# Kernel optimization log

Hardware: AMD Instinct MI355X
Metric: run time of the kernel (lower is better)

Reference implementation:

```python
import jax, jax.numpy as jnp
import numpy as np

B, T, C, M = 64, 1024, 256, 1024  # note: broadcast in the torch source forces M == T


def setup_inputs() -> dict:
    key = jax.random.key(0)
    k = jax.random.split(key, 6)
    x = jax.random.normal(k[0], (B, T, C), jnp.float32)
    memory = 0.02 * jax.random.normal(k[1], (1, M, C), jnp.float32)  # nn.init.normal_(std=0.02)
    w1 = jax.random.normal(k[2], (2 * C, 4 * C), jnp.float32) / np.sqrt(2 * C)
    b1 = jnp.zeros((4 * C,), jnp.float32)
    w2 = jax.random.normal(k[3], (4 * C, C), jnp.float32) / np.sqrt(4 * C)
    b2 = jnp.zeros((C,), jnp.float32)
    return {"x": x, "memory": memory, "w1": w1, "b1": b1, "w2": w2, "b2": b2}


def reference(x, memory, w1, b1, w2, b2):
    # x: [B,T,C], memory: [1,M,C] (shared across batch, expanded lazily)
    mem = memory[0]                                        # [M,C]
    energy = jnp.einsum('btc,mc->btm', x, mem)             # cross-attn scores
    weights = jax.nn.softmax(energy, axis=-1)              # [B,T,M]
    retrieved = jnp.einsum('btm,mc->btc', weights, mem)    # [B,T,C]
    cat = jnp.concatenate([x, retrieved], axis=-1)         # [B,T,2C] (forward output)
    # gate MLP: Linear(2C,4C) -> SiLU -> Linear(4C,C) -> Sigmoid
    h = jax.nn.silu(jnp.einsum('btk,kf->btf', cat, w1) + b1)
    update_gate = jax.nn.sigmoid(jnp.einsum('btf,fc->btc', h, w2) + b2)  # [B,T,C], T==M
    # memory blend + batch-mean reduction (side-effect update in torch, detached)
    x_mean = jnp.mean(x, axis=1, keepdims=True)            # [B,1,C]
    new_mem = memory * (1.0 - update_gate) + x_mean * update_gate  # [B,M,C]
    new_memory = jnp.mean(new_mem, axis=0, keepdims=True)  # [1,M,C]
    return cat, new_memory
```

## Files before the change

### kernel.cpp

```cpp
#include <hip/hip_runtime.h>
#include <hip/hip_bf16.h>


#define BT 65536

typedef short bf16x8 __attribute__((ext_vector_type(8)));
typedef float f32x4 __attribute__((ext_vector_type(4)));

__device__ __forceinline__ unsigned short f2bf(float f) {
    unsigned x = __float_as_uint(f);
    unsigned r = (x + 0x7FFFu + ((x >> 16) & 1u)) >> 16;
    return (unsigned short)r;
}
__device__ __forceinline__ float bf2f(unsigned short u) {
    return __uint_as_float(((unsigned)u) << 16);
}

__device__ __forceinline__ void async16(const unsigned short* g, unsigned short* l) {
    __builtin_amdgcn_global_load_lds((const __attribute__((address_space(1))) unsigned int*)g,
                                     (__attribute__((address_space(3))) unsigned int*)l,
                                     16, 0, 0);
}


__global__ __launch_bounds__(256) void prep_x(const float* __restrict__ x,
                                              float* __restrict__ cat_out,
                                              unsigned short* __restrict__ cat_b) {
    long tid = (long)blockIdx.x * 256 + threadIdx.x;
    long i4 = tid * 4;
    long row = i4 >> 8;
    int c = (int)(i4 & 255);
    float4 v = *(const float4*)&x[i4];
    *(float4*)&cat_out[row * 512 + c] = v;
    ushort4 b4;
    b4.x = f2bf(v.x); b4.y = f2bf(v.y); b4.z = f2bf(v.z); b4.w = f2bf(v.w);
    *(ushort4*)&cat_b[row * 512 + c] = b4;
}

__global__ __launch_bounds__(256) void prep_mem(const float* __restrict__ mem,
                                                unsigned short* __restrict__ mem_b,
                                                unsigned short* __restrict__ memT_b) {
    int tid = blockIdx.x * 256 + threadIdx.x;
    mem_b[tid] = f2bf(mem[tid]);
    int c = tid >> 10, m = tid & 1023;
    memT_b[tid] = f2bf(mem[m * 256 + c]);
}

__global__ __launch_bounds__(256) void prep_w1(const float* __restrict__ w1,
                                               unsigned short* __restrict__ w1T) {
    int tid = blockIdx.x * 256 + threadIdx.x;
    int f = tid >> 9, k = tid & 511;
    w1T[tid] = f2bf(w1[k * 1024 + f]);
}

__global__ __launch_bounds__(256) void prep_w2(const float* __restrict__ w2,
                                               unsigned short* __restrict__ w2T) {
    int tid = blockIdx.x * 256 + threadIdx.x;
    int c = tid >> 10, k = tid & 1023;
    w2T[tid] = f2bf(w2[k * 256 + c]);
}

__global__ __launch_bounds__(256) void xmean_k(const float* __restrict__ x,
                                               float* __restrict__ xmean) {
    int b = blockIdx.x;
    int t0 = blockIdx.y * 64;
    int c = threadIdx.x;
    float s = 0.f;
    for (int t = 0; t < 64; t++)
        s += x[((long)(b * 1024 + t0 + t)) * 256 + c];
    atomicAdd(&xmean[b * 256 + c], s * (1.f / 1024.f));
}


__device__ __forceinline__ void compute_tile(const unsigned short* bufA,
                                             const unsigned short* bufB,
                                             const int* aoff, const int* boff,
                                             f32x4 acc[4][4]) {
    bf16x8 af[4], bfr[4];
#pragma unroll
    for (int i = 0; i < 4; i++) af[i] = *(const bf16x8*)&bufA[aoff[i]];
#pragma unroll
    for (int j = 0; j < 4; j++) bfr[j] = *(const bf16x8*)&bufB[boff[j]];
#pragma unroll
    for (int i = 0; i < 4; i++)
#pragma unroll
        for (int j = 0; j < 4; j++)
            acc[i][j] = __builtin_amdgcn_mfma_f32_16x16x32_bf16(af[i], bfr[j], acc[i][j], 0, 0, 0);
}

template <int MODE, int K>
__global__ __launch_bounds__(256) void gemm_bt(const unsigned short* __restrict__ A,
                                               const unsigned short* __restrict__ Bt,
                                               float* __restrict__ outF,
                                               unsigned short* __restrict__ outB,
                                               const float* __restrict__ bias) {
    constexpr long LDA = (MODE == 0 || MODE == 2) ? 512 : 1024;
    constexpr int NK = K / 32;
    const int t = threadIdx.x;
    const int wave = t >> 6, lane = t & 63;
    const int waveM = wave >> 1, waveN = wave & 1;
    const int quad = lane >> 4, l16 = lane & 15;

    const int nwg = gridDim.x * gridDim.y;
    const int lid = blockIdx.y * gridDim.x + blockIdx.x;
    const int sid = (lid & 7) * (nwg >> 3) + (lid >> 3);
    const int nb = sid % gridDim.x;
    const int mb = sid / gridDim.x;
    const long n0 = (long)nb * 128;
    const long m0 = (long)mb * 128;

    __shared__ unsigned short lA[3][128 * 32];
    __shared__ unsigned short lB[3][128 * 32];

    f32x4 acc[4][4] = {};

    const int sRow = wave * 16 + (lane >> 2);
    const int sC = (lane & 3) ^ ((sRow >> 1) & 3);
    const unsigned short* Ag0 = A + (m0 + sRow) * LDA + sC * 8;
    const unsigned short* Ag1 = Ag0 + 64 * LDA;
    const unsigned short* Bg0 = Bt + (n0 + sRow) * (long)K + sC * 8;
    const unsigned short* Bg1 = Bg0 + 64 * (long)K;
    const int so0 = wave * 512;
    const int so1 = 2048 + wave * 512;

    const int sx = (l16 >> 1) & 3;
    int aoff[4], boff[4];
#pragma unroll
    for (int i = 0; i < 4; i++) {
        aoff[i] = (waveM * 64 + i * 16 + l16) * 32 + ((quad ^ sx) * 8);
        boff[i] = (waveN * 64 + i * 16 + l16) * 32 + ((quad ^ sx) * 8);
    }

#define STAGE(BUF, KT) do {                                   \
        async16(Ag0 + (KT) * 32, &lA[BUF][so0]);              \
        async16(Ag1 + (KT) * 32, &lA[BUF][so1]);              \
        async16(Bg0 + (KT) * 32, &lB[BUF][so0]);              \
        async16(Bg1 + (KT) * 32, &lB[BUF][so1]);              \
    } while (0)

    STAGE(0, 0);
    STAGE(1, 1);
    asm volatile("s_waitcnt vmcnt(4)" ::: "memory");
    __builtin_amdgcn_s_barrier();
    __builtin_amdgcn_sched_barrier(0);

#pragma unroll
    for (int kt = 0; kt < NK; ++kt) {
        if (kt + 2 < NK) {
            STAGE((kt + 2) % 3, kt + 2);
            __builtin_amdgcn_sched_barrier(0);
        }
        compute_tile(&lA[kt % 3][0], &lB[kt % 3][0], aoff, boff, acc);
        if (kt + 2 < NK) {
            asm volatile("s_waitcnt vmcnt(4) lgkmcnt(0)" ::: "memory");
            __builtin_amdgcn_s_barrier();
            __builtin_amdgcn_sched_barrier(0);
        } else if (kt + 1 < NK) {
            asm volatile("s_waitcnt vmcnt(0) lgkmcnt(0)" ::: "memory");
            __builtin_amdgcn_s_barrier();
            __builtin_amdgcn_sched_barrier(0);
        }
    }
#undef STAGE

#pragma unroll
    for (int i = 0; i < 4; i++) {
#pragma unroll
        for (int j = 0; j < 4; j++) {
            long col = n0 + waveN * 64 + j * 16 + l16;
            float bval = (MODE == 2 || MODE == 3) ? bias[col] : 0.f;
#pragma unroll
            for (int r = 0; r < 4; r++) {
                long row = m0 + waveM * 64 + i * 16 + quad * 4 + r;
                float v = acc[i][j][r];
                if (MODE == 0) {
                    outB[row * 1024 + col] = f2bf(v);
                } else if (MODE == 1) {
                    long o = row * 512 + 256 + col;
                    outF[o] = v;
                    outB[o] = f2bf(v);
                } else if (MODE == 2) {
                    float z = v + bval;
                    float s = 1.f / (1.f + __expf(-z));
                    outB[row * 1024 + col] = f2bf(z * s);
                } else {
                    float z = v + bval;
                    outF[row * 256 + col] = 1.f / (1.f + __expf(-z));
                }
            }
        }
    }
}

__global__ __launch_bounds__(256) void softmax_rows(unsigned short* __restrict__ P) {
    long row = (long)blockIdx.x * 4 + (threadIdx.x >> 6);
    int lane = threadIdx.x & 63;
    unsigned short* p = P + row * 1024 + lane * 16;
    uint4 u0 = *(const uint4*)p;
    uint4 u1 = *(const uint4*)(p + 8);
    const unsigned short* ua = (const unsigned short*)&u0;
    const unsigned short* ub = (const unsigned short*)&u1;
    float v[16];
#pragma unroll
    for (int i = 0; i < 8; i++) { v[i] = bf2f(ua[i]); v[i + 8] = bf2f(ub[i]); }
    float m = -1e30f;
#pragma unroll
    for (int i = 0; i < 16; i++) m = fmaxf(m, v[i]);
    for (int off = 32; off >= 1; off >>= 1) m = fmaxf(m, __shfl_xor(m, off));
    float s = 0.f;
#pragma unroll
    for (int i = 0; i < 16; i++) { v[i] = __expf(v[i] - m); s += v[i]; }
    for (int off = 32; off >= 1; off >>= 1) s += __shfl_xor(s, off);
    float inv = 1.f / s;
    unsigned short o[16];
#pragma unroll
    for (int i = 0; i < 16; i++) o[i] = f2bf(v[i] * inv);
    *(uint4*)p = *(uint4*)&o[0];
    *(uint4*)(p + 8) = *(uint4*)&o[8];
}

__global__ __launch_bounds__(256) void reduce_mem(const float* __restrict__ gate,
                                                  const float* __restrict__ memory,
                                                  const float* __restrict__ xmean,
                                                  float* __restrict__ out2) {
    int m = blockIdx.x, c = threadIdx.x;
    float mm = memory[m * 256 + c];
    float s = 0.f;
    for (int b = 0; b < 64; b++)
        s += gate[((long)(b * 1024 + m)) * 256 + c] * (xmean[b * 256 + c] - mm);
    out2[m * 256 + c] = mm + s * (1.f / 64.f);
}

extern "C" void kernel_launch(void* const* d_in, const int* in_sizes, int n_in,
                              void* d_out, int out_size, void* d_ws, size_t ws_size,
                              hipStream_t stream) {
    const float* x      = (const float*)d_in[0];
    const float* memory = (const float*)d_in[1];
    const float* w1     = (const float*)d_in[2];
    const float* b1     = (const float*)d_in[3];
    const float* w2     = (const float*)d_in[4];
    const float* b2     = (const float*)d_in[5];
    float* out = (float*)d_out;

    unsigned short* mem_b  = (unsigned short*)d_ws;
    unsigned short* memT_b = mem_b + 262144;
    unsigned short* w1T    = memT_b + 262144;
    unsigned short* w2T    = w1T + 524288;
    float* xmean           = (float*)(w2T + 262144);
    unsigned short* cat_b  = (unsigned short*)(xmean + 16384);
    unsigned short* Pbuf   = cat_b + 33554432;
    float* gate            = (float*)cat_b;

    hipMemsetAsync(xmean, 0, 64 * 256 * sizeof(float), stream);

    prep_mem<<<1024, 256, 0, stream>>>(memory, mem_b, memT_b);
    prep_w1<<<2048, 256, 0, stream>>>(w1, w1T);
    prep_w2<<<1024, 256, 0, stream>>>(w2, w2T);
    prep_x<<<16384, 256, 0, stream>>>(x, out, cat_b);
    xmean_k<<<dim3(64, 16), 256, 0, stream>>>(x, xmean);

    gemm_bt<0, 256><<<dim3(8, 512), 256, 0, stream>>>(cat_b, mem_b, nullptr, Pbuf, nullptr);
    softmax_rows<<<16384, 256, 0, stream>>>(Pbuf);
    gemm_bt<1, 1024><<<dim3(2, 512), 256, 0, stream>>>(Pbuf, memT_b, out, cat_b, nullptr);
    gemm_bt<2, 512><<<dim3(8, 512), 256, 0, stream>>>(cat_b, w1T, nullptr, Pbuf, b1);
    gemm_bt<3, 1024><<<dim3(2, 512), 256, 0, stream>>>(Pbuf, w2T, gate, nullptr, b2);

    reduce_mem<<<1024, 256, 0, stream>>>(gate, memory, xmean, out + 33554432);
}
```

Measured before the change: 550.9 us.

## Fuse energy GEMM with row softmax into one attention-score kernel

Replaces the separate energy GEMM and row-softmax kernels with one kernel in which each 512-thread block computes a full 64x1024 score tile in registers, streaming the memory matrix through double-buffered LDS. It does the row max and sum reduction across waves through shared memory and writes normalized bf16 probabilities once. This removes a full write and re-read of the 64K x 1024 bf16 score matrix and one launch. The cost is high register pressure (128 accumulators per lane), A fragments read directly from global memory, and scattered 2-byte stores.

Measured after the change: 575.4 us. +4.4%, slower.

```diff
diff --git a/kernel.cpp b/kernel.cpp
--- a/kernel.cpp
+++ b/kernel.cpp
@@ -20,6 +20,10 @@
     __builtin_amdgcn_global_load_lds((const __attribute__((address_space(1))) unsigned int*)g,
                                      (__attribute__((address_space(3))) unsigned int*)l,
                                      16, 0, 0);
+}
+
+__device__ __forceinline__ f32x4 mfma16(bf16x8 a, bf16x8 b, f32x4 c) {
+    return __builtin_amdgcn_mfma_f32_16x16x32_bf16(a, b, c, 0, 0, 0);
 }
 
 
@@ -71,6 +75,146 @@
     atomicAdd(&xmean[b * 256 + c], s * (1.f / 1024.f));
 }
 
+__global__ __launch_bounds__(512, 2) void attn_es(const unsigned short* __restrict__ catb,
+                                                  const unsigned short* __restrict__ memB,
+                                                  unsigned short* __restrict__ P) {
+    const int t = threadIdx.x;
+    const int wave = t >> 6, lane = t & 63;
+    const int quad = lane >> 4, l16 = lane & 15;
+    const long m0 = (long)blockIdx.x * 64;
+
+    __shared__ unsigned short lB[2][32768];
+
+    f32x4 acc[4][8] = {};
+
+    const int bRow = wave * 128 + (lane >> 2);
+    const int bChk = (lane & 3) ^ ((bRow >> 1) & 3);
+    const unsigned short* bSrc = memB + (long)bRow * 256 + bChk * 8;
+
+#define STAGE(BUF, KST) do { _Pragma("unroll")                                \
+    for (int j = 0; j < 8; j++)                                               \
+        async16(bSrc + (long)j * (16 * 256) + (KST) * 32,                     \
+                &lB[BUF][(wave * 128 + j * 16) * 32]); } while (0)
+
+    const unsigned short* Ap[4];
+#pragma unroll
+    for (int i = 0; i < 4; i++)
+        Ap[i] = catb + (m0 + i * 16 + l16) * 512 + quad * 8;
+
+    int boff[8];
+#pragma unroll
+    for (int n = 0; n < 8; n++) {
+        int r = wave * 128 + n * 16 + l16;
+        boff[n] = r * 32 + ((quad ^ ((r >> 1) & 3)) * 8);
+    }
+
+    STAGE(0, 0);
+#pragma unroll
+    for (int kst = 0; kst < 8; kst++) {
+        bf16x8 af[4];
+#pragma unroll
+        for (int i = 0; i < 4; i++) af[i] = *(const bf16x8*)(Ap[i] + kst * 32);
+        __builtin_amdgcn_sched_barrier(0);
+        if (kst < 7) STAGE((kst + 1) & 1, kst + 1);
+        __builtin_amdgcn_sched_barrier(0);
+        if (kst < 7) asm volatile("s_waitcnt vmcnt(8)" ::: "memory");
+        else         asm volatile("s_waitcnt vmcnt(0)" ::: "memory");
+        __builtin_amdgcn_sched_barrier(0);
+        const unsigned short* bb = &lB[kst & 1][0];
+        bf16x8 bfr[8];
+#pragma unroll
+        for (int n = 0; n < 8; n++) bfr[n] = *(const bf16x8*)&bb[boff[n]];
+#pragma unroll
+        for (int i = 0; i < 4; i++)
+#pragma unroll
+            for (int n = 0; n < 8; n++)
+                acc[i][n] = mfma16(af[i], bfr[n], acc[i][n]);
+    }
+#undef STAGE
+
+    f32x4 vmax[4];
+#pragma unroll
+    for (int m = 0; m < 4; m++) {
+        f32x4 v = acc[m][0];
+#pragma unroll
+        for (int n = 1; n < 8; n++)
+#pragma unroll
+            for (int r = 0; r < 4; r++) v[r] = fmaxf(v[r], acc[m][n][r]);
+#pragma unroll
+        for (int b = 1; b < 16; b <<= 1)
+#pragma unroll
+            for (int r = 0; r < 4; r++) v[r] = fmaxf(v[r], __shfl_xor(v[r], b));
+        vmax[m] = v;
+    }
+    __syncthreads();
+    float* red = (float*)&lB[0][0];
+    if (l16 == 0) {
+#pragma unroll
+        for (int m = 0; m < 4; m++)
+            *(f32x4*)&red[wave * 64 + m * 16 + quad * 4] = vmax[m];
+    }
+    __syncthreads();
+#pragma unroll
+    for (int m = 0; m < 4; m++) {
+        f32x4 v = *(const f32x4*)&red[m * 16 + quad * 4];
+#pragma unroll
+        for (int w = 1; w < 8; w++) {
+            f32x4 o = *(const f32x4*)&red[w * 64 + m * 16 + quad * 4];
+#pragma unroll
+            for (int r = 0; r < 4; r++) v[r] = fmaxf(v[r], o[r]);
+        }
+        vmax[m] = v;
+    }
+    f32x4 vsum[4];
+    float* red2 = red + 512;
+#pragma unroll
+    for (int m = 0; m < 4; m++) {
+        f32x4 s = {0.f, 0.f, 0.f, 0.f};
+#pragma unroll
+        for (int n = 0; n < 8; n++)
+#pragma unroll
+            for (int r = 0; r < 4; r++) {
+                float e = __expf(acc[m][n][r] - vmax[m][r]);
+                acc[m][n][r] = e;
+                s[r] += e;
+            }
+#pragma unroll
+        for (int b = 1; b < 16; b <<= 1)
+#pragma unroll
+            for (int r = 0; r < 4; r++) s[r] += __shfl_xor(s[r], b);
+        vsum[m] = s;
+    }
+    if (l16 == 0) {
+#pragma unroll
+        for (int m = 0; m < 4; m++)
+            *(f32x4*)&red2[wave * 64 + m * 16 + quad * 4] = vsum[m];
+    }
+    __syncthreads();
+#pragma unroll
+    for (int m = 0; m < 4; m++) {
+        f32x4 s = *(const f32x4*)&red2[m * 16 + quad * 4];
+#pragma unroll
+        for (int w = 1; w < 8; w++) {
+            f32x4 o = *(const f32x4*)&red2[w * 64 + m * 16 + quad * 4];
+#pragma unroll
+            for (int r = 0; r < 4; r++) s[r] += o[r];
+        }
+#pragma unroll
+        for (int r = 0; r < 4; r++) vsum[m][r] = 1.f / s[r];
+    }
+#pragma unroll
+    for (int m = 0; m < 4; m++)
+#pragma unroll
+        for (int n = 0; n < 8; n++) {
+            long col = wave * 128 + n * 16 + l16;
+#pragma unroll
+            for (int r = 0; r < 4; r++) {
+                long row = m0 + m * 16 + quad * 4 + r;
+                P[row * 1024 + col] = f2bf(acc[m][n][r] * vsum[m][r]);
+            }
+        }
+}
+
 
 __device__ __forceinline__ void compute_tile(const unsigned short* bufA,
                                              const unsigned short* bufB,
@@ -173,9 +317,7 @@
             for (int r = 0; r < 4; r++) {
                 long row = m0 + waveM * 64 + i * 16 + quad * 4 + r;
                 float v = acc[i][j][r];
-                if (MODE == 0) {
-                    outB[row * 1024 + col] = f2bf(v);
-                } else if (MODE == 1) {
+                if (MODE == 1) {
                     long o = row * 512 + 256 + col;
                     outF[o] = v;
                     outB[o] = f2bf(v);
@@ -192,33 +334,6 @@
     }
 }
 
-__global__ __launch_bounds__(256) void softmax_rows(unsigned short* __restrict__ P) {
-    long row = (long)blockIdx.x * 4 + (threadIdx.x >> 6);
-    int lane = threadIdx.x & 63;
-    unsigned short* p = P + row * 1024 + lane * 16;
-    uint4 u0 = *(const uint4*)p;
-    uint4 u1 = *(const uint4*)(p + 8);
-    const unsigned short* ua = (const unsigned short*)&u0;
-    const unsigned short* ub = (const unsigned short*)&u1;
-    float v[16];
-#pragma unroll
-    for (int i = 0; i < 8; i++) { v[i] = bf2f(ua[i]); v[i + 8] = bf2f(ub[i]); }
-    float m = -1e30f;
-#pragma unroll
-    for (int i = 0; i < 16; i++) m = fmaxf(m, v[i]);
-    for (int off = 32; off >= 1; off >>= 1) m = fmaxf(m, __shfl_xor(m, off));
-    float s = 0.f;
-#pragma unroll
-    for (int i = 0; i < 16; i++) { v[i] = __expf(v[i] - m); s += v[i]; }
-    for (int off = 32; off >= 1; off >>= 1) s += __shfl_xor(s, off);
-    float inv = 1.f / s;
-    unsigned short o[16];
-#pragma unroll
-    for (int i = 0; i < 16; i++) o[i] = f2bf(v[i] * inv);
-    *(uint4*)p = *(uint4*)&o[0];
-    *(uint4*)(p + 8) = *(uint4*)&o[8];
-}
-
 __global__ __launch_bounds__(256) void reduce_mem(const float* __restrict__ gate,
                                                   const float* __restrict__ memory,
                                                   const float* __restrict__ xmean,
@@ -259,8 +374,7 @@
     prep_x<<<16384, 256, 0, stream>>>(x, out, cat_b);
     xmean_k<<<dim3(64, 16), 256, 0, stream>>>(x, xmean);
 
-    gemm_bt<0, 256><<<dim3(8, 512), 256, 0, stream>>>(cat_b, mem_b, nullptr, Pbuf, nullptr);
-    softmax_rows<<<16384, 256, 0, stream>>>(Pbuf);
+    attn_es<<<1024, 512, 0, stream>>>(cat_b, mem_b, Pbuf);
     gemm_bt<1, 1024><<<dim3(2, 512), 256, 0, stream>>>(Pbuf, memT_b, out, cat_b, nullptr);
     gemm_bt<2, 512><<<dim3(8, 512), 256, 0, stream>>>(cat_b, w1T, nullptr, Pbuf, b1);
     gemm_bt<3, 1024><<<dim3(2, 512), 256, 0, stream>>>(Pbuf, w2T, gate, nullptr, b2);
```
